# Performance work log

Hardware: AMD Instinct MI355X
Metric: run time of the kernel (lower is better)

## Reference

```python
import jax, jax.numpy as jnp
import numpy as np

RANK = 16
ALPHA = 32
SCALING = ALPHA / RANK  # alpha / rank


def setup_inputs() -> dict:
    key = jax.random.key(0)
    k_x, k_w, k_b, k_a, k_bb = jax.random.split(key, 5)
    B, S, D_IN, D_OUT = 4, 2048, 4096, 4096
    x = jax.random.normal(k_x, (B, S, D_IN), dtype=jnp.float32)
    W = jax.random.normal(k_w, (D_OUT, D_IN), dtype=jnp.float32) * (1.0 / np.sqrt(D_IN))
    b = jax.random.normal(k_b, (D_OUT,), dtype=jnp.float32) * 0.02
    # LoRA init: A ~ N(0, 2/rank); B is zeros in the module, but we use small
    # random values so the adapter path is numerically exercised.
    lora_A = jax.random.normal(k_a, (RANK, D_IN), dtype=jnp.float32) * np.sqrt(2.0 / RANK)
    lora_B = jax.random.normal(k_bb, (D_OUT, RANK), dtype=jnp.float32) * 0.02
    return {"x": x, "W": W, "b": b, "lora_A": lora_A, "lora_B": lora_B}


def reference(x, W, b, lora_A, lora_B):
    # Base linear: x @ W^T + b
    base = jnp.einsum("bsd,od->bso", x, W) + b
    # LoRA path, fused as two rank-r matmuls (never materializing B@A):
    # (x @ A^T) @ B^T * scaling  ==  F.linear(x, B@A) * scaling
    xa = jnp.einsum("bsd,rd->bsr", x, lora_A)      # [B,S,r]
    lora = jnp.einsum("bsr,or->bso", xa, lora_B)    # [B,S,D_out]
    return base + lora * SCALING
```

## Files before the change

kernel.cpp:

```cpp
#include <hip/hip_runtime.h>
#include <hip/hip_bf16.h>

#define K_DIM 4096
#define N_DIM 4096
#define R_DIM 16
#define SCALING_F 2.0f

#define BM 256
#define BN 256
#define BK 64

#define FOLD_ROWS 8
#define FOLD_BLOCKS (N_DIM / FOLD_ROWS)

typedef __attribute__((ext_vector_type(8))) short bf16x8;
typedef __attribute__((ext_vector_type(4))) float f32x4;

__device__ __forceinline__ ushort f2bf(float f) {
  union { float f; unsigned u; } v; v.f = f;
  unsigned u = v.u;
  u += 0x7FFF + ((u >> 16) & 1);
  return (ushort)(u >> 16);
}

__global__ __launch_bounds__(256) void prepass_kernel(
    const float* __restrict__ x, ushort* __restrict__ xb,
    const float* __restrict__ W, const float* __restrict__ A,
    const float* __restrict__ Bl, ushort* __restrict__ wb, long n4) {
  if (blockIdx.x < FOLD_BLOCKS) {
    const int o0 = blockIdx.x * FOLD_ROWS;
#pragma unroll 1
    for (int j = 0; j < 4; ++j) {
      const int d0 = (threadIdx.x + j * 256) * 4;
      float4 a[R_DIM];
#pragma unroll
      for (int r = 0; r < R_DIM; ++r)
        a[r] = *(const float4*)(A + (size_t)r * K_DIM + d0);
#pragma unroll 1
      for (int rr = 0; rr < FOLD_ROWS; ++rr) {
        const int o = o0 + rr;
        float4 w = *(const float4*)(W + (size_t)o * K_DIM + d0);
        float s0 = w.x, s1 = w.y, s2 = w.z, s3 = w.w;
#pragma unroll
        for (int r = 0; r < R_DIM; ++r) {
          const float bv = Bl[o * R_DIM + r] * SCALING_F;
          s0 += bv * a[r].x; s1 += bv * a[r].y;
          s2 += bv * a[r].z; s3 += bv * a[r].w;
        }
        ushort4 ob;
        ob.x = f2bf(s0); ob.y = f2bf(s1); ob.z = f2bf(s2); ob.w = f2bf(s3);
        *(ushort4*)(wb + (size_t)o * K_DIM + d0) = ob;
      }
    }
  } else {
    long i = (long)(blockIdx.x - FOLD_BLOCKS) * blockDim.x + threadIdx.x;
    long stride = 2048L * blockDim.x;
    for (; i < n4; i += stride) {
      long idx = i * 4;
      float4 v = *(const float4*)(x + idx);
      ushort4 o;
      o.x = f2bf(v.x); o.y = f2bf(v.y); o.z = f2bf(v.z); o.w = f2bf(v.w);
      *(ushort4*)(xb + idx) = o;
    }
  }
}


#define RS 8192L

#define GLOAD(SRC, LOFF)                                                    \
  __builtin_amdgcn_global_load_lds(                                         \
      (const __attribute__((address_space(1))) void*)(SRC),                 \
      (__attribute__((address_space(3))) void*)(smem + (LOFF)), 16, 0, 0)

#define LDSA(BUF) ((BUF) * 32768)
#define LDSB(BUF) (65536 + (BUF) * 32768)

#define ST_A_EVEN(T, BUF) do {                                              \
    GLOAD(aS + (size_t)(T) * 128,            LDSA(BUF) + ldsDst);           \
    GLOAD(aS + (size_t)(T) * 128 + 128 * RS, LDSA(BUF) + 16384 + ldsDst); } while (0)
#define ST_A_ODD(T, BUF) do {                                               \
    GLOAD(aS + (size_t)(T) * 128 + 64 * RS,  LDSA(BUF) + 8192 + ldsDst);    \
    GLOAD(aS + (size_t)(T) * 128 + 192 * RS, LDSA(BUF) + 24576 + ldsDst); } while (0)
#define ST_B_H0(T, BUF) do {                                                \
    GLOAD(bS + (size_t)(T) * 128,            LDSB(BUF) + ldsDst);           \
    GLOAD(bS + (size_t)(T) * 128 + 64 * RS,  LDSB(BUF) + 8192 + ldsDst); } while (0)
#define ST_B_H1(T, BUF) do {                                                \
    GLOAD(bS + (size_t)(T) * 128 + 128 * RS, LDSB(BUF) + 16384 + ldsDst);   \
    GLOAD(bS + (size_t)(T) * 128 + 192 * RS, LDSB(BUF) + 24576 + ldsDst); } while (0)

#define LDA(M, CK, BUF) (*(const bf16x8*)(smem + LDSA(BUF) + aRd + (M) * 2048 + (CK)))
#define LDB(N, CK, BUF) (*(const bf16x8*)(smem + LDSB(BUF) + bRd + (N) * 2048 + (CK)))

#define PF_A8(MB, BUF) do {                                                 \
    afr[0][0] = LDA((MB) + 0, cK0, BUF); afr[0][1] = LDA((MB) + 0, cK1, BUF); \
    afr[1][0] = LDA((MB) + 1, cK0, BUF); afr[1][1] = LDA((MB) + 1, cK1, BUF); \
    afr[2][0] = LDA((MB) + 2, cK0, BUF); afr[2][1] = LDA((MB) + 2, cK1, BUF); \
    afr[3][0] = LDA((MB) + 3, cK0, BUF); afr[3][1] = LDA((MB) + 3, cK1, BUF); } while (0)

#define PF_B8(BUF) do {                                                     \
    bfr[0][0] = LDB(0, cK0, BUF); bfr[0][1] = LDB(0, cK1, BUF);             \
    bfr[1][0] = LDB(1, cK0, BUF); bfr[1][1] = LDB(1, cK1, BUF);             \
    bfr[2][0] = LDB(2, cK0, BUF); bfr[2][1] = LDB(2, cK1, BUF);             \
    bfr[3][0] = LDB(3, cK0, BUF); bfr[3][1] = LDB(3, cK1, BUF); } while (0)

#define MFMA32(MB) do {                                                     \
    _Pragma("unroll") for (int mm = 0; mm < 4; ++mm)                        \
      _Pragma("unroll") for (int nn = 0; nn < 4; ++nn) {                    \
        acc[(MB) + mm][nn] = __builtin_amdgcn_mfma_f32_16x16x32_bf16(       \
            afr[mm][0], bfr[nn][0], acc[(MB) + mm][nn], 0, 0, 0);           \
        acc[(MB) + mm][nn] = __builtin_amdgcn_mfma_f32_16x16x32_bf16(       \
            afr[mm][1], bfr[nn][1], acc[(MB) + mm][nn], 0, 0, 0); } } while (0)

#define PH_OPEN() do {                                                      \
    __builtin_amdgcn_s_barrier();                                           \
    asm volatile("s_waitcnt lgkmcnt(0)");                                   \
    __builtin_amdgcn_s_setprio(1); } while (0)

__global__ __launch_bounds__(512, 2) void gemm_lora_kernel(
    const ushort* __restrict__ Ab, const ushort* __restrict__ Bb,
    const float* __restrict__ bias, float* __restrict__ C) {
  __shared__ char smem[131072];

  const int tid = threadIdx.x;
  const int wave = tid >> 6, lane = tid & 63;
  const int wm = wave >> 2, wn = wave & 3;
  const int fr = lane & 15, fq = lane >> 4;

  const int bid = blockIdx.x;
  const int bm = ((bid & 7) << 2) + ((bid >> 3) & 3);
  const int bn = bid >> 5;

  const int trow = tid >> 3;
  const int tswz = ((tid & 7) << 4) ^ ((trow & 7) << 4);
  const char* aS = (const char*)Ab + (size_t)(bm * BM + trow) * RS + tswz;
  const char* bS = (const char*)Bb + (size_t)(bn * BN + trow) * RS + tswz;
  const int ldsDst = tid << 4;

  const int sa  = (fr & 7) << 4;
  const int cK0 = (fq << 4) ^ sa;
  const int cK1 = (64 | (fq << 4)) ^ sa;
  const int aRd = ((wm << 7) + fr) << 7;
  const int bRd = ((wn << 6) + fr) << 7;

  f32x4 acc[8][4];
#pragma unroll
  for (int m = 0; m < 8; ++m)
#pragma unroll
    for (int n = 0; n < 4; ++n) acc[m][n] = (f32x4){0.f, 0.f, 0.f, 0.f};
  bf16x8 afr[4][2], bfr[4][2];

  ST_B_H0(0, 0); ST_B_H1(0, 0); ST_A_EVEN(0, 0); ST_A_ODD(0, 0);
  ST_B_H0(1, 1); ST_B_H1(1, 1); ST_A_EVEN(1, 1);
  asm volatile("s_waitcnt vmcnt(6)" ::: "memory");
  __builtin_amdgcn_s_barrier();
  PF_B8(0);
  PF_A8(0, 0);

  const int NIT = K_DIM / (2 * BK);
#pragma unroll 1
  for (int i = 0; i < NIT; ++i) {
    const int t1 = 2 * i + 1, t2 = 2 * i + 2, t3 = 2 * i + 3;
    const bool last = (i == NIT - 1);

    ST_A_ODD(t1, 1);
    PH_OPEN();
    MFMA32(0);
    __builtin_amdgcn_s_setprio(0);
    PF_A8(4, 0);
    asm volatile("s_waitcnt vmcnt(2)" ::: "memory");
    __builtin_amdgcn_s_barrier();

    if (!last) { ST_B_H0(t2, 0); ST_B_H1(t2, 0); ST_A_EVEN(t2, 0); }
    PH_OPEN();
    MFMA32(4);
    __builtin_amdgcn_s_setprio(0);
    PF_B8(1);
    PF_A8(0, 1);
    if (last) asm volatile("s_waitcnt vmcnt(0)" ::: "memory");
    else      asm volatile("s_waitcnt vmcnt(6)" ::: "memory");
    __builtin_amdgcn_s_barrier();

    if (!last) ST_A_ODD(t2, 0);
    PH_OPEN();
    MFMA32(0);
    __builtin_amdgcn_s_setprio(0);
    PF_A8(4, 1);
    if (!last) asm volatile("s_waitcnt vmcnt(2)" ::: "memory");
    __builtin_amdgcn_s_barrier();

    if (!last) { ST_B_H0(t3, 1); ST_B_H1(t3, 1); ST_A_EVEN(t3, 1); }
    PH_OPEN();
    MFMA32(4);
    __builtin_amdgcn_s_setprio(0);
    if (!last) {
      PF_B8(0);
      PF_A8(0, 0);
      asm volatile("s_waitcnt vmcnt(6)" ::: "memory");
      __builtin_amdgcn_s_barrier();
    }
  }

  const int ccol0 = bn * BN + wn * 64 + fr;
  float bv[4];
#pragma unroll
  for (int n = 0; n < 4; ++n) bv[n] = bias[ccol0 + n * 16];
  const int crow0 = bm * BM + wm * 128 + fq * 4;
#pragma unroll
  for (int m = 0; m < 8; ++m)
#pragma unroll
    for (int n = 0; n < 4; ++n)
#pragma unroll
      for (int v = 0; v < 4; ++v) {
        int row = crow0 + m * 16 + v;
        C[(size_t)row * N_DIM + ccol0 + n * 16] = acc[m][n][v] + bv[n];
      }
}

extern "C" void kernel_launch(void* const* d_in, const int* in_sizes, int n_in,
                              void* d_out, int out_size, void* d_ws, size_t ws_size,
                              hipStream_t stream) {
  const float* x  = (const float*)d_in[0];
  const float* W  = (const float*)d_in[1];
  const float* b  = (const float*)d_in[2];
  const float* lA = (const float*)d_in[3];
  const float* lB = (const float*)d_in[4];
  float* out = (float*)d_out;

  const int M = in_sizes[0] / K_DIM;

  ushort* xb = (ushort*)d_ws;
  ushort* wb = xb + (size_t)M * K_DIM;

  long n4 = (long)M * K_DIM / 4;
  prepass_kernel<<<FOLD_BLOCKS + 2048, 256, 0, stream>>>(x, xb, W, lA, lB, wb, n4);
  gemm_lora_kernel<<<(M / BM) * (N_DIM / BN), 512, 0, stream>>>(xb, wb, b, out);
}
```

Measured before the change: 298.4 us.

## Interleave LDS fragment loads with MFMAs in finer-grained eight-phase pipeline

Splits each K-tile's compute into four phases, one per half-K slice and per M half, and issues the next fragment's LDS reads between MFMA groups instead of after the whole MFMA block. The A fragment register array is halved so fewer VGPRs are live, and the global loads are spread across more barrier phases with adjusted vmcnt waits. The aim is to hide LDS latency behind matrix work and cut register pressure. The cost is twice as many barriers per iteration and a more complex dependency schedule.

```diff
diff --git a/kernel.cpp b/kernel.cpp
--- a/kernel.cpp
+++ b/kernel.cpp
@@ -92,30 +92,43 @@
 #define LDA(M, CK, BUF) (*(const bf16x8*)(smem + LDSA(BUF) + aRd + (M) * 2048 + (CK)))
 #define LDB(N, CK, BUF) (*(const bf16x8*)(smem + LDSB(BUF) + bRd + (N) * 2048 + (CK)))
 
-#define PF_A8(MB, BUF) do {                                                 \
-    afr[0][0] = LDA((MB) + 0, cK0, BUF); afr[0][1] = LDA((MB) + 0, cK1, BUF); \
-    afr[1][0] = LDA((MB) + 1, cK0, BUF); afr[1][1] = LDA((MB) + 1, cK1, BUF); \
-    afr[2][0] = LDA((MB) + 2, cK0, BUF); afr[2][1] = LDA((MB) + 2, cK1, BUF); \
-    afr[3][0] = LDA((MB) + 3, cK0, BUF); afr[3][1] = LDA((MB) + 3, cK1, BUF); } while (0)
-
-#define PF_B8(BUF) do {                                                     \
-    bfr[0][0] = LDB(0, cK0, BUF); bfr[0][1] = LDB(0, cK1, BUF);             \
-    bfr[1][0] = LDB(1, cK0, BUF); bfr[1][1] = LDB(1, cK1, BUF);             \
-    bfr[2][0] = LDB(2, cK0, BUF); bfr[2][1] = LDB(2, cK1, BUF);             \
-    bfr[3][0] = LDB(3, cK0, BUF); bfr[3][1] = LDB(3, cK1, BUF); } while (0)
-
-#define MFMA32(MB) do {                                                     \
-    _Pragma("unroll") for (int mm = 0; mm < 4; ++mm)                        \
-      _Pragma("unroll") for (int nn = 0; nn < 4; ++nn) {                    \
-        acc[(MB) + mm][nn] = __builtin_amdgcn_mfma_f32_16x16x32_bf16(       \
-            afr[mm][0], bfr[nn][0], acc[(MB) + mm][nn], 0, 0, 0);           \
-        acc[(MB) + mm][nn] = __builtin_amdgcn_mfma_f32_16x16x32_bf16(       \
-            afr[mm][1], bfr[nn][1], acc[(MB) + mm][nn], 0, 0, 0); } } while (0)
-
-#define PH_OPEN() do {                                                      \
+#define MFMA1(MM, NN, KK)                                                   \
+  acc[MM][NN] = __builtin_amdgcn_mfma_f32_16x16x32_bf16(                    \
+      afr[(MM) & 3], bfr[NN][KK], acc[MM][NN], 0, 0, 0)
+
+#define PH_MMAJOR(MB, KK, NMB, NCK, NBUF) do {                              \
     __builtin_amdgcn_s_barrier();                                           \
     asm volatile("s_waitcnt lgkmcnt(0)");                                   \
-    __builtin_amdgcn_s_setprio(1); } while (0)
+    __builtin_amdgcn_s_setprio(1);                                          \
+    _Pragma("unroll") for (int mm = 0; mm < 4; ++mm) {                      \
+      MFMA1((MB) + mm, 0, KK); MFMA1((MB) + mm, 1, KK);                     \
+      MFMA1((MB) + mm, 2, KK); MFMA1((MB) + mm, 3, KK);                     \
+      afr[mm] = LDA((NMB) + mm, NCK, NBUF);                                 \
+    }                                                                       \
+    __builtin_amdgcn_s_setprio(0); } while (0)
+
+#define PH_NMAJOR(MB, KK, NBUF) do {                                        \
+    __builtin_amdgcn_s_barrier();                                           \
+    asm volatile("s_waitcnt lgkmcnt(0)");                                   \
+    __builtin_amdgcn_s_setprio(1);                                          \
+    _Pragma("unroll") for (int nn = 0; nn < 4; ++nn) {                      \
+      MFMA1((MB) + 0, nn, KK); MFMA1((MB) + 1, nn, KK);                     \
+      MFMA1((MB) + 2, nn, KK); MFMA1((MB) + 3, nn, KK);                     \
+      bfr[nn][0] = LDB(nn, cK0, NBUF); bfr[nn][1] = LDB(nn, cK1, NBUF);     \
+    }                                                                       \
+    afr[0] = LDA(0, cK0, NBUF); afr[1] = LDA(1, cK0, NBUF);                 \
+    afr[2] = LDA(2, cK0, NBUF); afr[3] = LDA(3, cK0, NBUF);                 \
+    __builtin_amdgcn_s_setprio(0); } while (0)
+
+#define PH_NMAJOR_TAIL(MB, KK) do {                                         \
+    __builtin_amdgcn_s_barrier();                                           \
+    asm volatile("s_waitcnt lgkmcnt(0)");                                   \
+    __builtin_amdgcn_s_setprio(1);                                          \
+    _Pragma("unroll") for (int nn = 0; nn < 4; ++nn) {                      \
+      MFMA1((MB) + 0, nn, KK); MFMA1((MB) + 1, nn, KK);                     \
+      MFMA1((MB) + 2, nn, KK); MFMA1((MB) + 3, nn, KK);                     \
+    }                                                                       \
+    __builtin_amdgcn_s_setprio(0); } while (0)
 
 __global__ __launch_bounds__(512, 2) void gemm_lora_kernel(
     const ushort* __restrict__ Ab, const ushort* __restrict__ Bb,
@@ -148,14 +161,16 @@
   for (int m = 0; m < 8; ++m)
 #pragma unroll
     for (int n = 0; n < 4; ++n) acc[m][n] = (f32x4){0.f, 0.f, 0.f, 0.f};
-  bf16x8 afr[4][2], bfr[4][2];
+  bf16x8 afr[4], bfr[4][2];
 
   ST_B_H0(0, 0); ST_B_H1(0, 0); ST_A_EVEN(0, 0); ST_A_ODD(0, 0);
   ST_B_H0(1, 1); ST_B_H1(1, 1); ST_A_EVEN(1, 1);
   asm volatile("s_waitcnt vmcnt(6)" ::: "memory");
   __builtin_amdgcn_s_barrier();
-  PF_B8(0);
-  PF_A8(0, 0);
+#pragma unroll
+  for (int n = 0; n < 4; ++n) { bfr[n][0] = LDB(n, cK0, 0); bfr[n][1] = LDB(n, cK1, 0); }
+#pragma unroll
+  for (int m = 0; m < 4; ++m) afr[m] = LDA(m, cK0, 0);
 
   const int NIT = K_DIM / (2 * BK);
 #pragma unroll 1
@@ -164,40 +179,42 @@
     const bool last = (i == NIT - 1);
 
     ST_A_ODD(t1, 1);
-    PH_OPEN();
-    MFMA32(0);
-    __builtin_amdgcn_s_setprio(0);
-    PF_A8(4, 0);
-    asm volatile("s_waitcnt vmcnt(2)" ::: "memory");
-    __builtin_amdgcn_s_barrier();
-
-    if (!last) { ST_B_H0(t2, 0); ST_B_H1(t2, 0); ST_A_EVEN(t2, 0); }
-    PH_OPEN();
-    MFMA32(4);
-    __builtin_amdgcn_s_setprio(0);
-    PF_B8(1);
-    PF_A8(0, 1);
+    PH_MMAJOR(0, 0, 0, cK1, 0);
+    __builtin_amdgcn_s_barrier();
+
+    if (!last) ST_B_H0(t2, 0);
+    PH_MMAJOR(0, 1, 4, cK0, 0);
+    __builtin_amdgcn_s_barrier();
+
+    if (!last) ST_B_H1(t2, 0);
+    PH_MMAJOR(4, 0, 4, cK1, 0);
     if (last) asm volatile("s_waitcnt vmcnt(0)" ::: "memory");
-    else      asm volatile("s_waitcnt vmcnt(6)" ::: "memory");
+    else      asm volatile("s_waitcnt vmcnt(4)" ::: "memory");
+    __builtin_amdgcn_s_barrier();
+
+    if (!last) ST_A_EVEN(t2, 0);
+    PH_NMAJOR(4, 1, 1);
     __builtin_amdgcn_s_barrier();
 
     if (!last) ST_A_ODD(t2, 0);
-    PH_OPEN();
-    MFMA32(0);
-    __builtin_amdgcn_s_setprio(0);
-    PF_A8(4, 1);
-    if (!last) asm volatile("s_waitcnt vmcnt(2)" ::: "memory");
-    __builtin_amdgcn_s_barrier();
-
-    if (!last) { ST_B_H0(t3, 1); ST_B_H1(t3, 1); ST_A_EVEN(t3, 1); }
-    PH_OPEN();
-    MFMA32(4);
-    __builtin_amdgcn_s_setprio(0);
+    PH_MMAJOR(0, 0, 0, cK1, 1);
+    __builtin_amdgcn_s_barrier();
+
+    if (!last) ST_B_H0(t3, 1);
+    PH_MMAJOR(0, 1, 4, cK0, 1);
+    __builtin_amdgcn_s_barrier();
+
+    if (!last) ST_B_H1(t3, 1);
+    PH_MMAJOR(4, 0, 4, cK1, 1);
+    if (!last) asm volatile("s_waitcnt vmcnt(4)" ::: "memory");
+    __builtin_amdgcn_s_barrier();
+
     if (!last) {
-      PF_B8(0);
-      PF_A8(0, 0);
-      asm volatile("s_waitcnt vmcnt(6)" ::: "memory");
+      ST_A_EVEN(t3, 1);
+      PH_NMAJOR(4, 1, 0);
       __builtin_amdgcn_s_barrier();
+    } else {
+      PH_NMAJOR_TAIL(4, 1);
     }
   }
 
```

Measured after the change: 1.030 ms. 245% more time.

## Split main loop into eight finer phases interleaving LDS reads with MFMAs

Applied to the files above, without the earlier changes.

Restructures the double-buffered GEMM loop from four coarse phases into eight half-K phases. Each phase issues 16 MFMAs while LDS fragment reads for the next phase are in flight, and it waits with a partial lgkmcnt instead of draining all LDS reads. B-fragment reloads are placed between MFMA columns. Register fragments shrink to two A sets and one B set, which relieves register pressure. The global prefetch order and vmcnt waits change to match. The cost is twice as many barriers per iteration and two full vmcnt(0) drains, which could hurt latency hiding.

```diff
diff --git a/kernel.cpp b/kernel.cpp
--- a/kernel.cpp
+++ b/kernel.cpp
@@ -92,30 +92,37 @@
 #define LDA(M, CK, BUF) (*(const bf16x8*)(smem + LDSA(BUF) + aRd + (M) * 2048 + (CK)))
 #define LDB(N, CK, BUF) (*(const bf16x8*)(smem + LDSB(BUF) + bRd + (N) * 2048 + (CK)))
 
-#define PF_A8(MB, BUF) do {                                                 \
-    afr[0][0] = LDA((MB) + 0, cK0, BUF); afr[0][1] = LDA((MB) + 0, cK1, BUF); \
-    afr[1][0] = LDA((MB) + 1, cK0, BUF); afr[1][1] = LDA((MB) + 1, cK1, BUF); \
-    afr[2][0] = LDA((MB) + 2, cK0, BUF); afr[2][1] = LDA((MB) + 2, cK1, BUF); \
-    afr[3][0] = LDA((MB) + 3, cK0, BUF); afr[3][1] = LDA((MB) + 3, cK1, BUF); } while (0)
-
-#define PF_B8(BUF) do {                                                     \
-    bfr[0][0] = LDB(0, cK0, BUF); bfr[0][1] = LDB(0, cK1, BUF);             \
-    bfr[1][0] = LDB(1, cK0, BUF); bfr[1][1] = LDB(1, cK1, BUF);             \
-    bfr[2][0] = LDB(2, cK0, BUF); bfr[2][1] = LDB(2, cK1, BUF);             \
-    bfr[3][0] = LDB(3, cK0, BUF); bfr[3][1] = LDB(3, cK1, BUF); } while (0)
-
-#define MFMA32(MB) do {                                                     \
-    _Pragma("unroll") for (int mm = 0; mm < 4; ++mm)                        \
-      _Pragma("unroll") for (int nn = 0; nn < 4; ++nn) {                    \
+#define RD_A(SET, MB, CK, BUF) do {                                         \
+    SET[0] = LDA((MB) + 0, CK, BUF); SET[1] = LDA((MB) + 1, CK, BUF);       \
+    SET[2] = LDA((MB) + 2, CK, BUF); SET[3] = LDA((MB) + 3, CK, BUF); } while (0)
+
+#define CL16(SET, MB) do {                                                  \
+    _Pragma("unroll") for (int nn = 0; nn < 4; ++nn)                        \
+      _Pragma("unroll") for (int mm = 0; mm < 4; ++mm)                      \
         acc[(MB) + mm][nn] = __builtin_amdgcn_mfma_f32_16x16x32_bf16(       \
-            afr[mm][0], bfr[nn][0], acc[(MB) + mm][nn], 0, 0, 0);           \
+            SET[mm], bfr[nn], acc[(MB) + mm][nn], 0, 0, 0); } while (0)
+
+#define CL16_BR(SET, MB, NCK, NBUF) do {                                    \
+    _Pragma("unroll") for (int nn = 0; nn < 4; ++nn) {                      \
+      _Pragma("unroll") for (int mm = 0; mm < 4; ++mm)                      \
         acc[(MB) + mm][nn] = __builtin_amdgcn_mfma_f32_16x16x32_bf16(       \
-            afr[mm][1], bfr[nn][1], acc[(MB) + mm][nn], 0, 0, 0); } } while (0)
-
-#define PH_OPEN() do {                                                      \
+            SET[mm], bfr[nn], acc[(MB) + mm][nn], 0, 0, 0);                 \
+      bfr[nn] = LDB(nn, NCK, NBUF);                                         \
+    } } while (0)
+
+#define PH_OPEN(N) do {                                                     \
     __builtin_amdgcn_s_barrier();                                           \
-    asm volatile("s_waitcnt lgkmcnt(0)");                                   \
+    asm volatile("s_waitcnt lgkmcnt(" #N ")");                              \
     __builtin_amdgcn_s_setprio(1); } while (0)
+
+#define PH_CLOSE() do {                                                     \
+    __builtin_amdgcn_s_setprio(0);                                          \
+    __builtin_amdgcn_s_barrier(); } while (0)
+
+#define PH_CLOSE_PUB() do {                                                 \
+    __builtin_amdgcn_s_setprio(0);                                          \
+    asm volatile("s_waitcnt vmcnt(0)" ::: "memory");                        \
+    __builtin_amdgcn_s_barrier(); } while (0)
 
 __global__ __launch_bounds__(512, 2) void gemm_lora_kernel(
     const ushort* __restrict__ Ab, const ushort* __restrict__ Bb,
@@ -148,14 +155,15 @@
   for (int m = 0; m < 8; ++m)
 #pragma unroll
     for (int n = 0; n < 4; ++n) acc[m][n] = (f32x4){0.f, 0.f, 0.f, 0.f};
-  bf16x8 afr[4][2], bfr[4][2];
+  bf16x8 afrA[4], afrB[4], bfr[4];
 
   ST_B_H0(0, 0); ST_B_H1(0, 0); ST_A_EVEN(0, 0); ST_A_ODD(0, 0);
-  ST_B_H0(1, 1); ST_B_H1(1, 1); ST_A_EVEN(1, 1);
+  ST_A_ODD(1, 1); ST_B_H0(1, 1); ST_B_H1(1, 1);
   asm volatile("s_waitcnt vmcnt(6)" ::: "memory");
   __builtin_amdgcn_s_barrier();
-  PF_B8(0);
-  PF_A8(0, 0);
+#pragma unroll
+  for (int n = 0; n < 4; ++n) bfr[n] = LDB(n, cK0, 0);
+  RD_A(afrB, 4, cK0, 0);
 
   const int NIT = K_DIM / (2 * BK);
 #pragma unroll 1
@@ -163,41 +171,54 @@
     const int t1 = 2 * i + 1, t2 = 2 * i + 2, t3 = 2 * i + 3;
     const bool last = (i == NIT - 1);
 
-    ST_A_ODD(t1, 1);
-    PH_OPEN();
-    MFMA32(0);
-    __builtin_amdgcn_s_setprio(0);
-    PF_A8(4, 0);
-    asm volatile("s_waitcnt vmcnt(2)" ::: "memory");
-    __builtin_amdgcn_s_barrier();
-
-    if (!last) { ST_B_H0(t2, 0); ST_B_H1(t2, 0); ST_A_EVEN(t2, 0); }
-    PH_OPEN();
-    MFMA32(4);
-    __builtin_amdgcn_s_setprio(0);
-    PF_B8(1);
-    PF_A8(0, 1);
-    if (last) asm volatile("s_waitcnt vmcnt(0)" ::: "memory");
-    else      asm volatile("s_waitcnt vmcnt(6)" ::: "memory");
-    __builtin_amdgcn_s_barrier();
-
-    if (!last) ST_A_ODD(t2, 0);
-    PH_OPEN();
-    MFMA32(0);
-    __builtin_amdgcn_s_setprio(0);
-    PF_A8(4, 1);
-    if (!last) asm volatile("s_waitcnt vmcnt(2)" ::: "memory");
-    __builtin_amdgcn_s_barrier();
-
-    if (!last) { ST_B_H0(t3, 1); ST_B_H1(t3, 1); ST_A_EVEN(t3, 1); }
-    PH_OPEN();
-    MFMA32(4);
-    __builtin_amdgcn_s_setprio(0);
+    RD_A(afrA, 0, cK0, 0);
+    ST_A_EVEN(t1, 1);
+    PH_OPEN(4);
+    CL16(afrB, 4);
+    PH_CLOSE();
+
+    RD_A(afrB, 4, cK1, 0);
+    PH_OPEN(4);
+    CL16_BR(afrA, 0, cK1, 0);
+    PH_CLOSE();
+
+    RD_A(afrA, 0, cK1, 0);
+    PH_OPEN(4);
+    CL16(afrB, 4);
+    PH_CLOSE_PUB();
+
+    RD_A(afrB, 4, cK0, 1);
+    if (!last) { ST_A_ODD(t2, 0); ST_B_H0(t2, 0); }
+    PH_OPEN(4);
+    CL16_BR(afrA, 0, cK0, 1);
+    PH_CLOSE();
+
+    RD_A(afrA, 0, cK0, 1);
+    if (!last) { ST_A_EVEN(t2, 0); ST_B_H1(t2, 0); }
+    PH_OPEN(4);
+    CL16(afrB, 4);
+    PH_CLOSE();
+
+    RD_A(afrB, 4, cK1, 1);
+    PH_OPEN(4);
+    CL16_BR(afrA, 0, cK1, 1);
+    PH_CLOSE();
+
+    RD_A(afrA, 0, cK1, 1);
+    PH_OPEN(4);
+    CL16(afrB, 4);
+    PH_CLOSE_PUB();
+
     if (!last) {
-      PF_B8(0);
-      PF_A8(0, 0);
-      asm volatile("s_waitcnt vmcnt(6)" ::: "memory");
-      __builtin_amdgcn_s_barrier();
+      RD_A(afrB, 4, cK0, 0);
+      ST_A_ODD(t3, 1); ST_B_H0(t3, 1); ST_B_H1(t3, 1);
+      PH_OPEN(4);
+      CL16_BR(afrA, 0, cK0, 0);
+      PH_CLOSE();
+    } else {
+      PH_OPEN(0);
+      CL16(afrA, 0);
+      __builtin_amdgcn_s_setprio(0);
     }
   }
 
```

Result: slower. 874.1 us (+192.9%).
